# Kernel tuning notes

Hardware: AMD Instinct MI355X
Metric: run time of the kernel (lower is better)

## Reference

```python
import jax, jax.numpy as jnp
import numpy as np

B, S, D = 2, 2048, 1024
H, KVH, HD = 16, 4, 64
ROPE_THETA = 10000.0


def rotate_half(x):
    h = x.shape[-1] // 2
    return jnp.concatenate([-x[..., h:], x[..., :h]], axis=-1)


def setup_inputs() -> dict:
    key = jax.random.key(0)
    k = jax.random.split(key, 6)
    x = jax.random.normal(k[0], (B, S, D), dtype=jnp.float32)
    # real RoPE tables: [S, HD//2]
    inv_freq = 1.0 / (ROPE_THETA ** (jnp.arange(0, HD, 2, dtype=jnp.float32) / HD))
    t = jnp.arange(S, dtype=jnp.float32)
    freqs = jnp.outer(t, inv_freq)  # [S, HD/2]
    cos = jnp.cos(freqs)
    sin = jnp.sin(freqs)
    # causal additive mask [1,1,S,S]
    neg = jnp.float32(-1e9)
    mask = jnp.where(jnp.tril(jnp.ones((S, S), dtype=bool)), 0.0, neg)[None, None]
    scale = 0.02
    wq = jax.random.normal(k[1], (D, H * HD), dtype=jnp.float32) * scale
    wk = jax.random.normal(k[2], (D, KVH * HD), dtype=jnp.float32) * scale
    wv = jax.random.normal(k[3], (D, KVH * HD), dtype=jnp.float32) * scale
    wo = jax.random.normal(k[4], (H * HD, D), dtype=jnp.float32) * scale
    return {"x": x, "cos": cos, "sin": sin, "mask": mask,
            "wq": wq, "wk": wk, "wv": wv, "wo": wo}


def reference(x, cos, sin, mask, wq, wk, wv, wo):
    b, s, d = x.shape
    hd = 2 * cos.shape[-1]
    h = wq.shape[1] // hd
    kvh = wk.shape[1] // hd
    n_rep = h // kvh

    q = (x @ wq).reshape(b, s, h, hd)
    k = (x @ wk).reshape(b, s, kvh, hd)
    v = (x @ wv).reshape(b, s, kvh, hd)

    # RoPE: cos/sin [S, hd/2] -> [1, s, 1, hd] via self-concat (rotate_half style)
    c = jnp.concatenate([cos[:s], cos[:s]], axis=-1)[None, :, None, :]
    sn = jnp.concatenate([sin[:s], sin[:s]], axis=-1)[None, :, None, :]
    q = q * c + rotate_half(q) * sn
    k = k * c + rotate_half(k) * sn

    new_k, new_v = k, v  # kv cache (pre-repeat)

    # GQA: repeat each kv head n_rep times contiguously (== expand+reshape)
    if n_rep > 1:
        k = jnp.repeat(k, n_rep, axis=2)
        v = jnp.repeat(v, n_rep, axis=2)

    scores = jnp.einsum('bqhd,bkhd->bhqk', q, k) / jnp.sqrt(jnp.float32(hd))
    scores = scores + mask
    attn = jax.nn.softmax(scores.astype(jnp.float32), axis=-1).astype(q.dtype)
    out = jnp.einsum('bhqk,bkhd->bqhd', attn, v).reshape(b, s, h * hd)
    out = out @ wo
    return (out, new_k, new_v)
```

## Files before the change

kernel.cpp:

```cpp
#include <hip/hip_runtime.h>
#include <hip/hip_bf16.h>

constexpr int B_ = 2, S_ = 2048, D_ = 1024, H_ = 16, KVH_ = 4, HD_ = 64;

typedef __attribute__((ext_vector_type(8))) short short8;
typedef __attribute__((ext_vector_type(4))) float f32x4;
typedef __attribute__((ext_vector_type(16))) float f32x16;

__device__ inline short f2b(float x) {
  unsigned u = __float_as_uint(x);
  return (short)((u + 0x7fffu + ((u >> 16) & 1u)) >> 16);
}
__device__ inline unsigned pkbf(float lo, float hi) {
  return ((unsigned)(unsigned short)f2b(hi) << 16) |
         (unsigned)(unsigned short)f2b(lo);
}

__device__ inline void async16(void* lds, const void* g) {
  __builtin_amdgcn_global_load_lds(
      (const __attribute__((address_space(1))) unsigned int*)g,
      (__attribute__((address_space(3))) unsigned int*)lds, 16, 0, 0);
}

__global__ __launch_bounds__(256) void cast_x_kernel(
    const float* __restrict__ x, short* __restrict__ xb) {
  int idx = (blockIdx.x * 256 + threadIdx.x) * 4;
  float4 v = *(const float4*)(x + idx);
  short4 o;
  o.x = f2b(v.x); o.y = f2b(v.y); o.z = f2b(v.z); o.w = f2b(v.w);
  *(short4*)(xb + idx) = o;
}

__global__ __launch_bounds__(256) void transpose_all_kernel(
    const float* __restrict__ wq, const float* __restrict__ wk,
    const float* __restrict__ wv, const float* __restrict__ wo,
    short* __restrict__ wt, short* __restrict__ wot) {
  const int z = blockIdx.z;
  const float* W;
  short* dst;
  int N;
  if (z == 0)      { W = wq; dst = wt;                       N = 1024; }
  else if (z == 1) { W = wo; dst = wot;                      N = 1024; }
  else if (z == 2) { W = wk; dst = wt + (size_t)1024 * 1024; N = 256; }
  else             { W = wv; dst = wt + (size_t)1280 * 1024; N = 256; }
  if (blockIdx.x * 64 >= N) return;

  __shared__ short ts[64][66];
  const int tid = threadIdx.x;
  const int bj = blockIdx.x, bi = blockIdx.y;
#pragma unroll
  for (int i = 0; i < 16; ++i) {
    int idx = tid + i * 256;
    int r = idx >> 6, c = idx & 63;
    ts[r][c] = f2b(W[(size_t)(bi * 64 + r) * N + bj * 64 + c]);
  }
  __syncthreads();
#pragma unroll
  for (int i = 0; i < 16; ++i) {
    int idx = tid + i * 256;
    int cc = idx >> 6, rr = idx & 63;
    dst[(size_t)(bj * 64 + cc) * 1024 + bi * 64 + rr] = ts[rr][cc];
  }
}

struct GemmLds {
  short As[128][32];
  short Bs[128][32];
};

__device__ inline void gemm_core(GemmLds& lds, const short* __restrict__ A,
                                 const short* __restrict__ Bt, int K, int row0,
                                 int col0, int tid, f32x4 (&acc)[4][4]) {
  const int w = tid >> 6, lane = tid & 63;
  const int grp = lane >> 4, li = lane & 15;
  const int wr = w & 1, wc = w >> 1;
  const int lr = lane >> 2, ls = (lane & 3) * 8;
#pragma unroll
  for (int mt = 0; mt < 4; ++mt)
#pragma unroll
    for (int nt = 0; nt < 4; ++nt) acc[mt][nt] = (f32x4){0.f, 0.f, 0.f, 0.f};

  for (int k0 = 0; k0 < K; k0 += 32) {
    __syncthreads();
#pragma unroll
    for (int i = 0; i < 2; ++i) {
      const int r = i * 64 + w * 16;
      async16(&lds.As[r][0], A + (size_t)(row0 + r + lr) * K + k0 + ls);
      async16(&lds.Bs[r][0], Bt + (size_t)(col0 + r + lr) * K + k0 + ls);
    }
    __syncthreads();

    short8 af[4], bf[4];
#pragma unroll
    for (int mt = 0; mt < 4; ++mt)
      af[mt] = *(const short8*)&lds.As[wr * 64 + mt * 16 + li][grp * 8];
#pragma unroll
    for (int nt = 0; nt < 4; ++nt)
      bf[nt] = *(const short8*)&lds.Bs[wc * 64 + nt * 16 + li][grp * 8];
#pragma unroll
    for (int mt = 0; mt < 4; ++mt)
#pragma unroll
      for (int nt = 0; nt < 4; ++nt)
        acc[mt][nt] = __builtin_amdgcn_mfma_f32_16x16x32_bf16(
            af[mt], bf[nt], acc[mt][nt], 0, 0, 0);
  }
}

__global__ __launch_bounds__(256) void gemm_qkv(
    const short* __restrict__ A, const short* __restrict__ Bt,
    const float* __restrict__ cs, const float* __restrict__ sn,
    short* __restrict__ qb, float* __restrict__ koutp, short* __restrict__ kb,
    float* __restrict__ voutp, short* __restrict__ vbT) {
  __shared__ GemmLds lds;
  const int tid = threadIdx.x;
  const int w = tid >> 6, lane = tid & 63;
  const int grp = lane >> 4, li = lane & 15;
  const int wr = w & 1, wc = w >> 1;
  const int row0 = blockIdx.y * 128, col0 = blockIdx.x * 128;
  f32x4 acc[4][4];
  gemm_core(lds, A, Bt, D_, row0, col0, tid, acc);

  if (col0 < 1024) {
#pragma unroll
    for (int mt = 0; mt < 4; ++mt)
#pragma unroll
      for (int r = 0; r < 4; ++r) {
        const int row = row0 + wr * 64 + mt * 16 + grp * 4 + r;
        const int spos = row & (S_ - 1);
#pragma unroll
        for (int nt = 0; nt < 2; ++nt) {
          const int col = col0 + wc * 64 + nt * 16 + li;
          const int d = col & 63;
          const float c = cs[spos * 32 + d];
          const float s = sn[spos * 32 + d];
          const float x0 = acc[mt][nt][r], x1 = acc[mt][nt + 2][r];
          qb[(size_t)row * 1024 + col] = f2b((x0 * c - x1 * s) * 0.125f);
          qb[(size_t)row * 1024 + col + 32] = f2b((x1 * c + x0 * s) * 0.125f);
        }
      }
  } else if (col0 < 1280) {
#pragma unroll
    for (int mt = 0; mt < 4; ++mt)
#pragma unroll
      for (int r = 0; r < 4; ++r) {
        const int row = row0 + wr * 64 + mt * 16 + grp * 4 + r;
        const int spos = row & (S_ - 1);
#pragma unroll
        for (int nt = 0; nt < 2; ++nt) {
          const int kcol = col0 + wc * 64 + nt * 16 + li - 1024;
          const int d = kcol & 63;
          const float c = cs[spos * 32 + d];
          const float s = sn[spos * 32 + d];
          const float x0 = acc[mt][nt][r], x1 = acc[mt][nt + 2][r];
          const float k0v = x0 * c - x1 * s;
          const float k1v = x1 * c + x0 * s;
          koutp[(size_t)row * 256 + kcol] = k0v;
          koutp[(size_t)row * 256 + kcol + 32] = k1v;
          kb[(size_t)row * 256 + kcol] = f2b(k0v);
          kb[(size_t)row * 256 + kcol + 32] = f2b(k1v);
        }
      }
  } else {
#pragma unroll
    for (int mt = 0; mt < 4; ++mt)
#pragma unroll
      for (int nt = 0; nt < 4; ++nt) {
        const int vcol = col0 + wc * 64 + nt * 16 + li - 1280;
        const int row_base = row0 + wr * 64 + mt * 16 + grp * 4;
        short4 pk;
        float vv[4];
#pragma unroll
        for (int r = 0; r < 4; ++r) vv[r] = acc[mt][nt][r];
        pk.x = f2b(vv[0]); pk.y = f2b(vv[1]);
        pk.z = f2b(vv[2]); pk.w = f2b(vv[3]);
#pragma unroll
        for (int r = 0; r < 4; ++r)
          voutp[(size_t)(row_base + r) * 256 + vcol] = vv[r];
        const int b = row_base >> 11, s0 = row_base & (S_ - 1);
        *(short4*)&vbT[((size_t)(b * 256 + vcol)) * S_ + s0] = pk;
      }
  }
}

struct KVT {
  short K[8][64][8];
  short V[8][64][8];
};

__global__ __launch_bounds__(256) void fattn_kernel(
    const short* __restrict__ qb, const short* __restrict__ kb,
    const short* __restrict__ vbT, short* __restrict__ o) {
  __shared__ KVT bufP[2][2];

  const int tid = threadIdx.x;
  const int w = tid >> 6, lane = tid & 63;
  const int n32 = lane & 31, kg = lane >> 5;
  const int st = w >> 1, par = w & 1;

  const int pr = blockIdx.x & 15;
  const int h = (blockIdx.x >> 4) & 15;
  const int b = blockIdx.x >> 8;
  const int kh = h >> 2;

  const short* kgp0 = kb + ((size_t)(b * S_) + lane) * 256 + kh * 64;
  const short* vgp0 = vbT + ((size_t)(b * 256 + kh * 64 + lane)) * S_;

  for (int pass = 0; pass < 2; ++pass) {
    const int qq = pass ? (31 - pr) : pr;
    const int nt = qq + 1, nph = (nt + 1) >> 1;
    const int qs0 = qq * 64 + st * 32;

    const short* qp =
        qb + (size_t)(b * S_ + qs0 + n32) * 1024 + h * 64 + kg * 8;
    short8 qa[4];
#pragma unroll
    for (int ks = 0; ks < 4; ++ks) qa[ks] = *(const short8*)(qp + ks * 16);

    f32x16 Oa0, Oa1;
#pragma unroll
    for (int i = 0; i < 16; ++i) { Oa0[i] = 0.f; Oa1[i] = 0.f; }
    float lreg = 0.f;

    auto issue = [&](int ph) {
      for (int tp = 0; tp < 2; ++tp) {
        const int t = 2 * ph + tp;
        if (t >= nt) break;
        KVT& d = bufP[ph & 1][tp];
        const short* kgp = kgp0 + (size_t)t * 16384;
        const short* vgp = vgp0 + t * 64;
        async16(&d.K[w][0][0], kgp + w * 8);
        async16(&d.K[w + 4][0][0], kgp + (w + 4) * 8);
        async16(&d.V[w][0][0], vgp + w * 8);
        async16(&d.V[w + 4][0][0], vgp + (w + 4) * 8);
      }
    };

    issue(0);
    for (int ph = 0; ph < nph; ++ph) {
      __syncthreads();
      if (ph + 1 < nph) issue(ph + 1);
      const int t = 2 * ph + par;
      if (t >= nt) continue;
      KVT& bf = bufP[ph & 1][par];
      const bool diag = (t == qq);

      unsigned pk[4][4];
#pragma unroll
      for (int s = 0; s < 2; ++s) {
        if (diag && st == 0 && s == 1) continue;
        f32x16 sv;
#pragma unroll
        for (int i = 0; i < 16; ++i) sv[i] = 0.f;
#pragma unroll
        for (int ks = 0; ks < 4; ++ks) {
          const short8 kf =
              *(const short8*)&bf.K[ks * 2 + kg][s * 32 + n32][0];
          sv = __builtin_amdgcn_mfma_f32_32x32x16_bf16(kf, qa[ks], sv, 0, 0, 0);
        }
        const bool dm = diag && (s == st);
        float p[16];
#pragma unroll
        for (int rr = 0; rr < 16; ++rr) {
          float e = __expf(sv[rr]);
          if (dm) {
            const int key32 = (rr & 3) + 8 * (rr >> 2) + 4 * kg;
            if (key32 > n32) e = 0.f;
          }
          p[rr] = e;
          lreg += e;
        }
        pk[2 * s][0] = pkbf(p[0], p[1]);
        pk[2 * s][1] = pkbf(p[2], p[3]);
        pk[2 * s][2] = pkbf(p[4], p[5]);
        pk[2 * s][3] = pkbf(p[6], p[7]);
        pk[2 * s + 1][0] = pkbf(p[8], p[9]);
        pk[2 * s + 1][1] = pkbf(p[10], p[11]);
        pk[2 * s + 1][2] = pkbf(p[12], p[13]);
        pk[2 * s + 1][3] = pkbf(p[14], p[15]);
      }

      const int kcmax = (diag && st == 0) ? 2 : 4;
      for (int kc = 0; kc < kcmax; ++kc) {
        const unsigned a0 = pk[kc][0], a1 = pk[kc][1];
        const unsigned b0 = pk[kc][2], b1 = pk[kc][3];
        const unsigned xa0 = (unsigned)__shfl_xor((int)a0, 32);
        const unsigned xa1 = (unsigned)__shfl_xor((int)a1, 32);
        const unsigned xb0 = (unsigned)__shfl_xor((int)b0, 32);
        const unsigned xb1 = (unsigned)__shfl_xor((int)b1, 32);
        union { unsigned u[4]; short8 s8; } f;
        f.u[0] = kg ? xb0 : a0;
        f.u[1] = kg ? xb1 : a1;
        f.u[2] = kg ? b0 : xa0;
        f.u[3] = kg ? b1 : xa1;
        const short8 v0 = *(const short8*)&bf.V[kc * 2 + kg][n32][0];
        const short8 v1 = *(const short8*)&bf.V[kc * 2 + kg][32 + n32][0];
        Oa0 = __builtin_amdgcn_mfma_f32_32x32x16_bf16(v0, f.s8, Oa0, 0, 0, 0);
        Oa1 = __builtin_amdgcn_mfma_f32_32x32x16_bf16(v1, f.s8, Oa1, 0, 0, 0);
      }
    }

    lreg += __shfl_xor(lreg, 32);

    __syncthreads();
    float* scr = (float*)&bufP[0][0];
    float* lb = (float*)((char*)&bufP[0][0] + 16384);
    if (par == 1) {
#pragma unroll
      for (int rr = 0; rr < 16; ++rr) {
        const int d = (rr & 3) + 8 * (rr >> 2) + 4 * kg;
        scr[(st * 64 + d) * 32 + n32] = Oa0[rr];
        scr[(st * 64 + d + 32) * 32 + n32] = Oa1[rr];
      }
      if (kg == 0) lb[st * 32 + n32] = lreg;
    }
    __syncthreads();
    if (par == 0) {
      const float inv = 1.0f / (lreg + lb[st * 32 + n32]);
#pragma unroll
      for (int rr = 0; rr < 16; ++rr) {
        const int d = (rr & 3) + 8 * (rr >> 2) + 4 * kg;
        scr[(st * 64 + d) * 32 + n32] =
            (Oa0[rr] + scr[(st * 64 + d) * 32 + n32]) * inv;
        scr[(st * 64 + d + 32) * 32 + n32] =
            (Oa1[rr] + scr[(st * 64 + d + 32) * 32 + n32]) * inv;
      }
    }
    __syncthreads();
    {
      const int ql = tid >> 2, dseg = (tid & 3) * 16;
      const size_t gb = (size_t)(b * S_ + qq * 64 + ql) * 1024 + h * 64 + dseg;
      short8 t0, t1;
#pragma unroll
      for (int k2 = 0; k2 < 8; ++k2) {
        t0[k2] = f2b(scr[((ql >> 5) * 64 + dseg + k2) * 32 + (ql & 31)]);
        t1[k2] = f2b(scr[((ql >> 5) * 64 + dseg + 8 + k2) * 32 + (ql & 31)]);
      }
      *(short8*)(o + gb) = t0;
      *(short8*)(o + gb + 8) = t1;
    }
    __syncthreads();
  }
}

__global__ __launch_bounds__(256) void gemm_bt_f32(
    const short* __restrict__ A, const short* __restrict__ Bt,
    float* __restrict__ C, int N, int K) {
  __shared__ GemmLds lds;
  const int tid = threadIdx.x;
  const int w = tid >> 6, lane = tid & 63;
  const int grp = lane >> 4, li = lane & 15;
  const int wr = w & 1, wc = w >> 1;
  const int row0 = blockIdx.y * 128, col0 = blockIdx.x * 128;
  f32x4 acc[4][4];
  gemm_core(lds, A, Bt, K, row0, col0, tid, acc);
#pragma unroll
  for (int mt = 0; mt < 4; ++mt)
#pragma unroll
    for (int nt = 0; nt < 4; ++nt)
#pragma unroll
      for (int r = 0; r < 4; ++r)
        C[(size_t)(row0 + wr * 64 + mt * 16 + grp * 4 + r) * N + col0 +
          wc * 64 + nt * 16 + li] = acc[mt][nt][r];
}

extern "C" void kernel_launch(void* const* d_in, const int* in_sizes, int n_in,
                              void* d_out, int out_size, void* d_ws,
                              size_t ws_size, hipStream_t stream) {
  const float* x  = (const float*)d_in[0];
  const float* cs = (const float*)d_in[1];
  const float* sn = (const float*)d_in[2];
  const float* wq = (const float*)d_in[4];
  const float* wk = (const float*)d_in[5];
  const float* wv = (const float*)d_in[6];
  const float* wo = (const float*)d_in[7];

  float* outp  = (float*)d_out;
  float* koutp = outp + (size_t)B_ * S_ * H_ * HD_;
  float* voutp = koutp + (size_t)B_ * S_ * KVH_ * HD_;

  char* p = (char*)d_ws;
  short* xb   = (short*)p; p += (size_t)B_ * S_ * D_ * 2;
  short* qb   = (short*)p; p += (size_t)B_ * S_ * H_ * HD_ * 2;
  short* kb   = (short*)p; p += (size_t)B_ * S_ * KVH_ * HD_ * 2;
  short* vbT  = (short*)p; p += (size_t)B_ * S_ * KVH_ * HD_ * 2;
  short* abuf = (short*)p; p += (size_t)B_ * S_ * H_ * HD_ * 2;
  short* wt   = (short*)p; p += (size_t)1536 * D_ * 2;
  short* wot  = (short*)p; p += (size_t)D_ * H_ * HD_ * 2;

  const int M = B_ * S_;

  cast_x_kernel<<<(M * D_) / 1024, 256, 0, stream>>>(x, xb);
  transpose_all_kernel<<<dim3(16, 16, 4), 256, 0, stream>>>(wq, wk, wv, wo,
                                                            wt, wot);

  gemm_qkv<<<dim3(1536 / 128, M / 128), 256, 0, stream>>>(
      xb, wt, cs, sn, qb, koutp, kb, voutp, vbT);

  fattn_kernel<<<B_ * H_ * 16, 256, 0, stream>>>(qb, kb, vbT, abuf);

  gemm_bt_f32<<<dim3(1024 / 128, M / 128), 256, 0, stream>>>(abuf, wot, outp,
                                                             1024, 1024);
}
```

Baseline: 202.3 us.

## Double-buffer GEMM LDS loads, fuse prep kernels, use exp2 softmax and packed bf16

```diff
diff --git a/kernel.cpp b/kernel.cpp
--- a/kernel.cpp
+++ b/kernel.cpp
@@ -11,9 +11,9 @@
   unsigned u = __float_as_uint(x);
   return (short)((u + 0x7fffu + ((u >> 16) & 1u)) >> 16);
 }
-__device__ inline unsigned pkbf(float lo, float hi) {
-  return ((unsigned)(unsigned short)f2b(hi) << 16) |
-         (unsigned)(unsigned short)f2b(lo);
+__device__ inline unsigned pkbf2(float lo, float hi) {
+  __hip_bfloat162 h = __float22bfloat162_rn(float2{lo, hi});
+  return *(unsigned*)&h;
 }
 
 __device__ inline void async16(void* lds, const void* g) {
@@ -22,20 +22,23 @@
       (__attribute__((address_space(3))) unsigned int*)lds, 16, 0, 0);
 }
 
-__global__ __launch_bounds__(256) void cast_x_kernel(
-    const float* __restrict__ x, short* __restrict__ xb) {
-  int idx = (blockIdx.x * 256 + threadIdx.x) * 4;
-  float4 v = *(const float4*)(x + idx);
-  short4 o;
-  o.x = f2b(v.x); o.y = f2b(v.y); o.z = f2b(v.z); o.w = f2b(v.w);
-  *(short4*)(xb + idx) = o;
-}
-
-__global__ __launch_bounds__(256) void transpose_all_kernel(
+__global__ __launch_bounds__(256) void prep_kernel(
+    const float* __restrict__ x, short* __restrict__ xb,
     const float* __restrict__ wq, const float* __restrict__ wk,
     const float* __restrict__ wv, const float* __restrict__ wo,
     short* __restrict__ wt, short* __restrict__ wot) {
-  const int z = blockIdx.z;
+  __shared__ short ts[64][66];
+  const int tid = threadIdx.x;
+  if (blockIdx.x < 4096) {
+    const int idx = (blockIdx.x * 256 + tid) * 4;
+    float4 v = *(const float4*)(x + idx);
+    short4 o;
+    o.x = f2b(v.x); o.y = f2b(v.y); o.z = f2b(v.z); o.w = f2b(v.w);
+    *(short4*)(xb + idx) = o;
+    return;
+  }
+  const int bid = blockIdx.x - 4096;
+  const int z = bid >> 8, bi = (bid >> 4) & 15, bj = bid & 15;
   const float* W;
   short* dst;
   int N;
@@ -43,11 +46,7 @@
   else if (z == 1) { W = wo; dst = wot;                      N = 1024; }
   else if (z == 2) { W = wk; dst = wt + (size_t)1024 * 1024; N = 256; }
   else             { W = wv; dst = wt + (size_t)1280 * 1024; N = 256; }
-  if (blockIdx.x * 64 >= N) return;
-
-  __shared__ short ts[64][66];
-  const int tid = threadIdx.x;
-  const int bj = blockIdx.x, bi = blockIdx.y;
+  if (bj * 64 >= N) return;
 #pragma unroll
   for (int i = 0; i < 16; ++i) {
     int idx = tid + i * 256;
@@ -63,14 +62,15 @@
   }
 }
 
-struct GemmLds {
-  short As[128][32];
-  short Bs[128][32];
+struct GemmLdsDb {
+  short As[2][128][32];
+  short Bs[2][128][32];
 };
 
-__device__ inline void gemm_core(GemmLds& lds, const short* __restrict__ A,
-                                 const short* __restrict__ Bt, int K, int row0,
-                                 int col0, int tid, f32x4 (&acc)[4][4]) {
+__device__ inline void gemm_core_db(GemmLdsDb& lds, const short* __restrict__ A,
+                                    const short* __restrict__ Bt, int K,
+                                    int row0, int col0, int tid,
+                                    f32x4 (&acc)[4][4]) {
   const int w = tid >> 6, lane = tid & 63;
   const int grp = lane >> 4, li = lane & 15;
   const int wr = w & 1, wc = w >> 1;
@@ -80,23 +80,29 @@
 #pragma unroll
     for (int nt = 0; nt < 4; ++nt) acc[mt][nt] = (f32x4){0.f, 0.f, 0.f, 0.f};
 
-  for (int k0 = 0; k0 < K; k0 += 32) {
-    __syncthreads();
+  auto issue = [&](int bi, int k0) {
 #pragma unroll
     for (int i = 0; i < 2; ++i) {
       const int r = i * 64 + w * 16;
-      async16(&lds.As[r][0], A + (size_t)(row0 + r + lr) * K + k0 + ls);
-      async16(&lds.Bs[r][0], Bt + (size_t)(col0 + r + lr) * K + k0 + ls);
+      async16(&lds.As[bi][r][0], A + (size_t)(row0 + r + lr) * K + k0 + ls);
+      async16(&lds.Bs[bi][r][0], Bt + (size_t)(col0 + r + lr) * K + k0 + ls);
     }
+  };
+
+  issue(0, 0);
+  const int nk = K >> 5;
+  for (int kk = 0; kk < nk; ++kk) {
+    const int cur = kk & 1;
     __syncthreads();
+    if (kk + 1 < nk) issue(cur ^ 1, (kk + 1) << 5);
 
     short8 af[4], bf[4];
 #pragma unroll
     for (int mt = 0; mt < 4; ++mt)
-      af[mt] = *(const short8*)&lds.As[wr * 64 + mt * 16 + li][grp * 8];
+      af[mt] = *(const short8*)&lds.As[cur][wr * 64 + mt * 16 + li][grp * 8];
 #pragma unroll
     for (int nt = 0; nt < 4; ++nt)
-      bf[nt] = *(const short8*)&lds.Bs[wc * 64 + nt * 16 + li][grp * 8];
+      bf[nt] = *(const short8*)&lds.Bs[cur][wc * 64 + nt * 16 + li][grp * 8];
 #pragma unroll
     for (int mt = 0; mt < 4; ++mt)
 #pragma unroll
@@ -105,20 +111,22 @@
             af[mt], bf[nt], acc[mt][nt], 0, 0, 0);
   }
 }
+
+#define QSCALE 0.1803368801111f
 
 __global__ __launch_bounds__(256) void gemm_qkv(
     const short* __restrict__ A, const short* __restrict__ Bt,
     const float* __restrict__ cs, const float* __restrict__ sn,
     short* __restrict__ qb, float* __restrict__ koutp, short* __restrict__ kb,
     float* __restrict__ voutp, short* __restrict__ vbT) {
-  __shared__ GemmLds lds;
+  __shared__ GemmLdsDb lds;
   const int tid = threadIdx.x;
   const int w = tid >> 6, lane = tid & 63;
   const int grp = lane >> 4, li = lane & 15;
   const int wr = w & 1, wc = w >> 1;
   const int row0 = blockIdx.y * 128, col0 = blockIdx.x * 128;
   f32x4 acc[4][4];
-  gemm_core(lds, A, Bt, D_, row0, col0, tid, acc);
+  gemm_core_db(lds, A, Bt, D_, row0, col0, tid, acc);
 
   if (col0 < 1024) {
 #pragma unroll
@@ -134,8 +142,8 @@
           const float c = cs[spos * 32 + d];
           const float s = sn[spos * 32 + d];
           const float x0 = acc[mt][nt][r], x1 = acc[mt][nt + 2][r];
-          qb[(size_t)row * 1024 + col] = f2b((x0 * c - x1 * s) * 0.125f);
-          qb[(size_t)row * 1024 + col + 32] = f2b((x1 * c + x0 * s) * 0.125f);
+          qb[(size_t)row * 1024 + col] = f2b((x0 * c - x1 * s) * QSCALE);
+          qb[(size_t)row * 1024 + col + 32] = f2b((x1 * c + x0 * s) * QSCALE);
         }
       }
   } else if (col0 < 1280) {
@@ -261,7 +269,7 @@
         float p[16];
 #pragma unroll
         for (int rr = 0; rr < 16; ++rr) {
-          float e = __expf(sv[rr]);
+          float e = exp2f(sv[rr]);
           if (dm) {
             const int key32 = (rr & 3) + 8 * (rr >> 2) + 4 * kg;
             if (key32 > n32) e = 0.f;
@@ -269,18 +277,17 @@
           p[rr] = e;
           lreg += e;
         }
-        pk[2 * s][0] = pkbf(p[0], p[1]);
-        pk[2 * s][1] = pkbf(p[2], p[3]);
-        pk[2 * s][2] = pkbf(p[4], p[5]);
-        pk[2 * s][3] = pkbf(p[6], p[7]);
-        pk[2 * s + 1][0] = pkbf(p[8], p[9]);
-        pk[2 * s + 1][1] = pkbf(p[10], p[11]);
-        pk[2 * s + 1][2] = pkbf(p[12], p[13]);
-        pk[2 * s + 1][3] = pkbf(p[14], p[15]);
-      }
-
-      const int kcmax = (diag && st == 0) ? 2 : 4;
-      for (int kc = 0; kc < kcmax; ++kc) {
+        pk[2 * s][0] = pkbf2(p[0], p[1]);
+        pk[2 * s][1] = pkbf2(p[2], p[3]);
+        pk[2 * s][2] = pkbf2(p[4], p[5]);
+        pk[2 * s][3] = pkbf2(p[6], p[7]);
+        pk[2 * s + 1][0] = pkbf2(p[8], p[9]);
+        pk[2 * s + 1][1] = pkbf2(p[10], p[11]);
+        pk[2 * s + 1][2] = pkbf2(p[12], p[13]);
+        pk[2 * s + 1][3] = pkbf2(p[14], p[15]);
+      }
+
+      auto pv = [&](int kc) {
         const unsigned a0 = pk[kc][0], a1 = pk[kc][1];
         const unsigned b0 = pk[kc][2], b1 = pk[kc][3];
         const unsigned xa0 = (unsigned)__shfl_xor((int)a0, 32);
@@ -296,6 +303,12 @@
         const short8 v1 = *(const short8*)&bf.V[kc * 2 + kg][32 + n32][0];
         Oa0 = __builtin_amdgcn_mfma_f32_32x32x16_bf16(v0, f.s8, Oa0, 0, 0, 0);
         Oa1 = __builtin_amdgcn_mfma_f32_32x32x16_bf16(v1, f.s8, Oa1, 0, 0, 0);
+      };
+      if (diag && st == 0) {
+        pv(0); pv(1);
+      } else {
+#pragma unroll
+        for (int kc = 0; kc < 4; ++kc) pv(kc);
       }
     }
 
@@ -345,14 +358,14 @@
 __global__ __launch_bounds__(256) void gemm_bt_f32(
     const short* __restrict__ A, const short* __restrict__ Bt,
     float* __restrict__ C, int N, int K) {
-  __shared__ GemmLds lds;
+  __shared__ GemmLdsDb lds;
   const int tid = threadIdx.x;
   const int w = tid >> 6, lane = tid & 63;
   const int grp = lane >> 4, li = lane & 15;
   const int wr = w & 1, wc = w >> 1;
   const int row0 = blockIdx.y * 128, col0 = blockIdx.x * 128;
   f32x4 acc[4][4];
-  gemm_core(lds, A, Bt, K, row0, col0, tid, acc);
+  gemm_core_db(lds, A, Bt, K, row0, col0, tid, acc);
 #pragma unroll
   for (int mt = 0; mt < 4; ++mt)
 #pragma unroll
@@ -389,9 +402,8 @@
 
   const int M = B_ * S_;
 
-  cast_x_kernel<<<(M * D_) / 1024, 256, 0, stream>>>(x, xb);
-  transpose_all_kernel<<<dim3(16, 16, 4), 256, 0, stream>>>(wq, wk, wv, wo,
-                                                            wt, wot);
+  prep_kernel<<<4096 + 1024, 256, 0, stream>>>(x, xb, wq, wk, wv, wo, wt,
+                                               wot);
 
   gemm_qkv<<<dim3(1536 / 128, M / 128), 256, 0, stream>>>(
       xb, wt, cs, sn, qb, koutp, kb, voutp, vbT);
```

After: 191.1 us. 5.5% less time.
